# Optimization experiments

Hardware: AMD Instinct MI355X
Metric: run time of the kernel (lower is better)

Reference implementation:

```python
import jax, jax.numpy as jnp
import numpy as np

UNITS = 2048
RHO = 0.99          # spectral_radius
LEAKY = 1.0         # leaky integration coefficient
INPUT_SCALING = 1.0
BIAS_SCALING = 1.0
B, T, D_IN = 32, 512, 128


def setup_inputs() -> dict:
    key = jax.random.key(0)
    k1, k2, k3 = jax.random.split(key, 3)
    inputs = jax.random.normal(k1, (B, T, D_IN), dtype=jnp.float32)
    h0 = jnp.zeros((B, UNITS), dtype=jnp.float32)
    # original uses deterministic +/-1 signs from pi digits; same structure: sign matrix * scaling
    kernel = jnp.where(jax.random.uniform(k2, (D_IN, UNITS)) >= 0.5, 1.0, -1.0).astype(jnp.float32) * INPUT_SCALING
    bias = jnp.where(jax.random.uniform(k3, (UNITS,)) >= 0.5, 1.0, -1.0).astype(jnp.float32) * BIAS_SCALING
    return {"inputs": inputs, "h0": h0, "kernel": kernel, "bias": bias}


def reference(inputs, h0, kernel, bias):
    # Precompute input projection for all timesteps: [B, T, U]
    u = jnp.einsum("btd,du->btu", inputs, kernel)

    def step(h, u_t):
        # prev @ recurrent_kernel == spectral_radius * cyclic shift of prev
        state_part = RHO * jnp.roll(h, 1, axis=-1)
        h_new = h * (1.0 - LEAKY) + jnp.tanh(u_t + bias + state_part) * LEAKY
        return h_new, h_new

    _, ys = jax.lax.scan(step, h0, jnp.swapaxes(u, 0, 1))  # scan over time
    return jnp.swapaxes(ys, 0, 1)  # [B, T, U]
```

## Files before the change

### kernel.cpp

```cpp
#include <hip/hip_runtime.h>
#include <hip/hip_bf16.h>

#define U_ 2048
#define T_ 512
#define K_ 128
#define B_ 32
#define RHO_ 0.99f
#define CPB 128
#define NTILES 9
#define NSLOTS 10

typedef __attribute__((ext_vector_type(8))) short short8;
typedef __attribute__((ext_vector_type(4))) float f32x4;

__device__ __forceinline__ unsigned short bf16_rne(float x) {
  unsigned int u = __float_as_uint(x);
  u += 0x7FFFu + ((u >> 16) & 1u);
  return (unsigned short)(u >> 16);
}

#define GLOAD_LDS16(gsrc, ldst)                                        \
  __builtin_amdgcn_global_load_lds(                                    \
      (const __attribute__((address_space(1))) void*)(gsrc),           \
      (__attribute__((address_space(3))) void*)(ldst), 16, 0, 0)

__global__ __launch_bounds__(256) void convert_a_kernel(
    const float* __restrict__ A, unsigned short* __restrict__ Ab) {
  const int gi = blockIdx.x * 256 + threadIdx.x;
  const int m = gi >> 5;
  const int kq = (gi & 31) << 2;
  const float4 v = *(const float4*)&A[(size_t)m * K_ + kq];
  ushort4 hi, lo;
  hi.x = bf16_rne(v.x); hi.y = bf16_rne(v.y); hi.z = bf16_rne(v.z); hi.w = bf16_rne(v.w);
  lo.x = bf16_rne(v.x - __uint_as_float((unsigned)hi.x << 16));
  lo.y = bf16_rne(v.y - __uint_as_float((unsigned)hi.y << 16));
  lo.z = bf16_rne(v.z - __uint_as_float((unsigned)hi.z << 16));
  lo.w = bf16_rne(v.w - __uint_as_float((unsigned)hi.w << 16));
  *(ushort4*)&Ab[(size_t)m * 256 + kq] = hi;
  *(ushort4*)&Ab[(size_t)m * 256 + 128 + kq] = lo;
}

__global__ __launch_bounds__(256) void convert_w_kernel(
    const float* __restrict__ W, unsigned short* __restrict__ Wbt) {
  const int gi = blockIdx.x * 256 + threadIdx.x;
  const int kq = gi >> 11;
  const int n = gi & 2047;
  const int k = kq << 2;
  ushort4 w;
  w.x = bf16_rne(W[(size_t)(k + 0) * U_ + n]);
  w.y = bf16_rne(W[(size_t)(k + 1) * U_ + n]);
  w.z = bf16_rne(W[(size_t)(k + 2) * U_ + n]);
  w.w = bf16_rne(W[(size_t)(k + 3) * U_ + n]);
  *(ushort4*)&Wbt[(size_t)n * 256 + k] = w;
  *(ushort4*)&Wbt[(size_t)n * 256 + 128 + k] = w;
}

__global__ __launch_bounds__(256, 2) void fused_gemm_scan5_kernel(
    const unsigned short* __restrict__ Ab, const unsigned short* __restrict__ Wbt,
    const float* __restrict__ bias, const float* __restrict__ h0,
    float* __restrict__ out) {
  __shared__ unsigned short Wl[NSLOTS * 2048];
  __shared__ unsigned short Al[2][4096];
  __shared__ float u_lds[2][16 * 146];
  const int tid = threadIdx.x;
  const int id = blockIdx.x + (blockIdx.y << 4);
  const int xcd = id & 7;
  const int wk = id >> 3;
  const int b = (xcd << 2) + (wk >> 4);
  const int bx = wk & 15;
  const int c0 = bx << 7;
  const int cbase = bx << 3;
  const int wave = tid >> 6;
  const int lane = tid & 63;
  const int r = lane & 15;
  const int q = lane >> 4;

  const unsigned short* const aBase = Ab + (((size_t)b * T_) << 8);

  if (tid < 128) {
    #pragma unroll
    for (int k = 0; k < 4; ++k) {
      const int p = tid + (k << 7);
      const int row = p >> 5, pg = p & 31;
      GLOAD_LDS16(aBase + ((size_t)row << 8) + ((pg ^ (row & 7)) << 3),
                  &Al[0][p << 3]);
    }
    #pragma unroll
    for (int j = 0; j < NTILES; ++j) {
      const int g = (cbase + j) & 127;
      #pragma unroll
      for (int k = 0; k < 2; ++k) {
        const int p = tid + (k << 7);
        const int row = p >> 4, pg = p & 15;
        GLOAD_LDS16(Wbt + ((size_t)((g << 4) + row) << 8) + ((pg ^ (row & 7)) << 3),
                    &Wl[(j << 11) + (p << 3)]);
      }
    }
  }
  float bv[3], nbv[3];
  bv[0] = bias[(c0 + (wave << 4) + r) & (U_ - 1)];
  bv[1] = bias[(c0 + ((wave + 4) << 4) + r) & (U_ - 1)];
  bv[2] = (wave == 2) ? bias[(c0 + 128 + r) & (U_ - 1)] : 0.0f;
  float h_prev = 0.0f;
  if (tid < CPB)
    h_prev = h0[((size_t)b << 11) + ((c0 + tid + U_ - 1) & (U_ - 1))];
  float hreg[16];

  __syncthreads();

  for (int it = 0; it < T_ / 16; ++it) {
    const int cur = it & 1;
    const int t0 = it << 4;

    if (tid < 128 && it + 1 < T_ / 16) {
      #pragma unroll
      for (int k = 0; k < 4; ++k) {
        const int p = tid + (k << 7);
        const int row = p >> 5, pg = p & 31;
        GLOAD_LDS16(aBase + ((size_t)(t0 + 16 + row) << 8) + ((pg ^ (row & 7)) << 3),
                    &Al[cur ^ 1][p << 3]);
      }
      const int g = (cbase + it + NTILES) & 127;
      const int snew = (it + NTILES) % NSLOTS;
      #pragma unroll
      for (int k = 0; k < 2; ++k) {
        const int p = tid + (k << 7);
        const int row = p >> 4, pg = p & 15;
        GLOAD_LDS16(Wbt + ((size_t)((g << 4) + row) << 8) + ((pg ^ (row & 7)) << 3),
                    &Wl[(snew << 11) + (p << 3)]);
      }
    }
    if (it + 1 < T_ / 16) {
      nbv[0] = bias[(c0 + t0 + 16 + (wave << 4) + r) & (U_ - 1)];
      nbv[1] = bias[(c0 + t0 + 16 + ((wave + 4) << 4) + r) & (U_ - 1)];
      if (wave == 2) nbv[2] = bias[(c0 + t0 + 16 + 128 + r) & (U_ - 1)];
    }
    __builtin_amdgcn_sched_barrier(0);

    if (tid < CPB && it > 0) {
      const int t0p = t0 - 16;
      float* const orow = out + (((size_t)(b * T_ + t0p)) << 11);
      #pragma unroll
      for (int tt = 0; tt < 16; ++tt)
        __builtin_nontemporal_store(
            hreg[tt], &orow[((size_t)tt << 11) + ((c0 + tid + t0p + tt) & (U_ - 1))]);
    }

    short8 af[8];
    #pragma unroll
    for (int ks = 0; ks < 8; ++ks)
      af[ks] = *(const short8*)&Al[cur][(r << 8) + ((((ks << 2) + q) ^ (r & 7)) << 3)];

    #pragma unroll
    for (int u = 0; u < 3; ++u) {
      const int j = (u < 2) ? (wave + (u << 2)) : 8;
      if (u < 2 || wave == 2) {
        const int slot = (it + j) % NSLOTS;
        short8 bfk[4];
        #pragma unroll
        for (int ks = 0; ks < 4; ++ks)
          bfk[ks] = *(const short8*)&Wl[(slot << 11) + (r << 7) +
                                        ((((ks << 2) + q) ^ (r & 7)) << 3)];
        f32x4 acc = (f32x4){0.f, 0.f, 0.f, 0.f};
        #pragma unroll
        for (int ks = 0; ks < 8; ++ks)
          acc = __builtin_amdgcn_mfma_f32_16x16x32_bf16(af[ks], bfk[ks & 3], acc, 0, 0, 0);
        #pragma unroll
        for (int reg = 0; reg < 4; ++reg)
          u_lds[cur][((q << 2) + reg) * 146 + (j << 4) + r] = acc[reg] + bv[u];
      }
    }

    asm volatile("s_waitcnt vmcnt(16) lgkmcnt(0)\n\ts_barrier" ::: "memory");
    __builtin_amdgcn_sched_barrier(0);

    if (tid < CPB) {
      float uv[16];
      #pragma unroll
      for (int tt = 0; tt < 16; ++tt)
        uv[tt] = u_lds[cur][tt * 146 + tid + tt];
      float x = fmaf(RHO_, h_prev, uv[0]);
      #pragma unroll
      for (int tt = 0; tt < 16; ++tt) {
        float e = __builtin_amdgcn_exp2f(2.8853900817779268f * x);
        float rc = __builtin_amdgcn_rcpf(e + 1.0f);
        hreg[tt] = fmaf(-2.0f, rc, 1.0f);
        if (tt < 15) x = fmaf(-2.0f * RHO_, rc, uv[tt + 1] + RHO_);
      }
      h_prev = hreg[15];
    }
    bv[0] = nbv[0]; bv[1] = nbv[1]; bv[2] = nbv[2];
  }

  if (tid < CPB) {
    const int t0p = T_ - 16;
    float* const orow = out + (((size_t)(b * T_ + t0p)) << 11);
    #pragma unroll
    for (int tt = 0; tt < 16; ++tt)
      __builtin_nontemporal_store(
          hreg[tt], &orow[((size_t)tt << 11) + ((c0 + tid + t0p + tt) & (U_ - 1))]);
  }
}

__device__ __forceinline__ float fast_tanh(float x) {
  float e = __builtin_amdgcn_exp2f(2.8853900817779268f * x);
  return 1.0f - 2.0f * __builtin_amdgcn_rcpf(e + 1.0f);
}

__global__ __launch_bounds__(256) void ring_scan_kernel(
    float* __restrict__ buf, const float* __restrict__ h0) {
  const int b = blockIdx.y;
  const int c = (blockIdx.x << 8) + threadIdx.x;
  float* const base = buf + (size_t)b * (T_ * U_);
  float h = h0[((size_t)b << 11) + ((c + U_ - 1) & (U_ - 1))];
  float wA[8], wB[8];
  #pragma unroll
  for (int j = 0; j < 8; ++j)
    wA[j] = base[((size_t)j << 11) + ((c + j) & (U_ - 1))];
  for (int t0 = 0; t0 < T_; t0 += 16) {
    #pragma unroll
    for (int j = 0; j < 8; ++j) {
      const int t = t0 + 8 + j;
      wB[j] = base[((size_t)t << 11) + ((c + t) & (U_ - 1))];
    }
    #pragma unroll
    for (int j = 0; j < 8; ++j) {
      const int t = t0 + j;
      h = fast_tanh(fmaf(RHO_, h, wA[j]));
      base[((size_t)t << 11) + ((c + t) & (U_ - 1))] = h;
    }
    if (t0 + 16 < T_) {
      #pragma unroll
      for (int j = 0; j < 8; ++j) {
        const int t = t0 + 16 + j;
        wA[j] = base[((size_t)t << 11) + ((c + t) & (U_ - 1))];
      }
    }
    #pragma unroll
    for (int j = 0; j < 8; ++j) {
      const int t = t0 + 8 + j;
      h = fast_tanh(fmaf(RHO_, h, wB[j]));
      base[((size_t)t << 11) + ((c + t) & (U_ - 1))] = h;
    }
  }
}

__global__ __launch_bounds__(256, 4) void gemm_bias_kernel(
    const float* __restrict__ A, const float* __restrict__ W,
    const float* __restrict__ bias, float* __restrict__ out) {
  __shared__ float Asf[64][68];
  __shared__ float Bsf[64][64];
  const int tid = threadIdx.x;
  const int m0 = blockIdx.y << 6;
  const int n0 = blockIdx.x << 6;
  const int tx = tid & 15;
  const int ty = tid >> 4;
  float acc[4][4] = {};
  #pragma unroll
  for (int kb = 0; kb < 2; ++kb) {
    if (kb) __syncthreads();
    {
      const int c4 = tid & 15;
      const int r0 = tid >> 4;
      #pragma unroll
      for (int rr = 0; rr < 4; ++rr) {
        const int r = r0 + (rr << 4);
        const float4 v = *(const float4*)(A + (size_t)(m0 + r) * K_ + (kb << 6) + (c4 << 2));
        Asf[(c4 << 2) + 0][r] = v.x;
        Asf[(c4 << 2) + 1][r] = v.y;
        Asf[(c4 << 2) + 2][r] = v.z;
        Asf[(c4 << 2) + 3][r] = v.w;
      }
    }
    {
      const int c4 = tid & 15;
      const int r0 = tid >> 4;
      #pragma unroll
      for (int rr = 0; rr < 4; ++rr) {
        const int k = r0 + (rr << 4);
        *(float4*)&Bsf[k][c4 << 2] =
            *(const float4*)(W + (size_t)((kb << 6) + k) * U_ + n0 + (c4 << 2));
      }
    }
    __syncthreads();
    #pragma unroll 16
    for (int k = 0; k < 64; ++k) {
      const float4 a = *(const float4*)&Asf[k][ty << 2];
      const float4 b = *(const float4*)&Bsf[k][tx << 2];
      acc[0][0] = fmaf(a.x, b.x, acc[0][0]); acc[0][1] = fmaf(a.x, b.y, acc[0][1]);
      acc[0][2] = fmaf(a.x, b.z, acc[0][2]); acc[0][3] = fmaf(a.x, b.w, acc[0][3]);
      acc[1][0] = fmaf(a.y, b.x, acc[1][0]); acc[1][1] = fmaf(a.y, b.y, acc[1][1]);
      acc[1][2] = fmaf(a.y, b.z, acc[1][2]); acc[1][3] = fmaf(a.y, b.w, acc[1][3]);
      acc[2][0] = fmaf(a.z, b.x, acc[2][0]); acc[2][1] = fmaf(a.z, b.y, acc[2][1]);
      acc[2][2] = fmaf(a.z, b.z, acc[2][2]); acc[2][3] = fmaf(a.z, b.w, acc[2][3]);
      acc[3][0] = fmaf(a.w, b.x, acc[3][0]); acc[3][1] = fmaf(a.w, b.y, acc[3][1]);
      acc[3][2] = fmaf(a.w, b.z, acc[3][2]); acc[3][3] = fmaf(a.w, b.w, acc[3][3]);
    }
  }
  const float4 bv = *(const float4*)(bias + n0 + (tx << 2));
  #pragma unroll
  for (int i = 0; i < 4; ++i) {
    float4 o;
    o.x = acc[i][0] + bv.x; o.y = acc[i][1] + bv.y;
    o.z = acc[i][2] + bv.z; o.w = acc[i][3] + bv.w;
    *(float4*)(out + (size_t)(m0 + (ty << 2) + i) * U_ + n0 + (tx << 2)) = o;
  }
}

extern "C" void kernel_launch(void* const* d_in, const int* in_sizes, int n_in,
                              void* d_out, int out_size, void* d_ws, size_t ws_size,
                              hipStream_t stream) {
  const float* A    = (const float*)d_in[0];
  const float* h0   = (const float*)d_in[1];
  const float* W    = (const float*)d_in[2];
  const float* bias = (const float*)d_in[3];
  float* out = (float*)d_out;

  const size_t AB_BYTES = (size_t)B_ * T_ * 256 * 2;
  const size_t WB_BYTES = (size_t)U_ * 256 * 2;
  const size_t NEEDED = AB_BYTES + WB_BYTES;

  if (ws_size >= NEEDED) {
    unsigned short* Ab  = (unsigned short*)d_ws;
    unsigned short* Wbt = (unsigned short*)((char*)d_ws + AB_BYTES);

    convert_a_kernel<<<2048, 256, 0, stream>>>(A, Ab);
    convert_w_kernel<<<256, 256, 0, stream>>>(W, Wbt);
    dim3 fg(U_ / CPB, B_);
    fused_gemm_scan5_kernel<<<fg, 256, 0, stream>>>(Ab, Wbt, bias, h0, out);
  } else {
    dim3 gemm_grid(U_ / 64, (B_ * T_) / 64);
    gemm_bias_kernel<<<gemm_grid, 256, 0, stream>>>(A, W, bias, out);
    dim3 scan_grid(U_ / 256, B_);
    ring_scan_kernel<<<scan_grid, 256, 0, stream>>>(out, h0);
  }
}
```

Before: 193.4 us.

## Split fused GEMM-scan kernel into producer and consumer waves

```diff
diff --git a/kernel.cpp b/kernel.cpp
--- a/kernel.cpp
+++ b/kernel.cpp
@@ -9,6 +9,7 @@
 #define CPB 128
 #define NTILES 9
 #define NSLOTS 10
+#define NIT (T_ / 16)
 
 typedef __attribute__((ext_vector_type(8))) short short8;
 typedef __attribute__((ext_vector_type(4))) float f32x4;
@@ -55,7 +56,7 @@
   *(ushort4*)&Wbt[(size_t)n * 256 + 128 + k] = w;
 }
 
-__global__ __launch_bounds__(256, 2) void fused_gemm_scan5_kernel(
+__global__ __launch_bounds__(256, 2) void fused_gemm_scan6_kernel(
     const unsigned short* __restrict__ Ab, const unsigned short* __restrict__ Wbt,
     const float* __restrict__ bias, const float* __restrict__ h0,
     float* __restrict__ out) {
@@ -74,13 +75,15 @@
   const int lane = tid & 63;
   const int r = lane & 15;
   const int q = lane >> 4;
+  const bool producer = (wave >= 2);
+  const int ptid = tid & 127;
 
   const unsigned short* const aBase = Ab + (((size_t)b * T_) << 8);
 
-  if (tid < 128) {
+  if (producer) {
     #pragma unroll
     for (int k = 0; k < 4; ++k) {
-      const int p = tid + (k << 7);
+      const int p = ptid + (k << 7);
       const int row = p >> 5, pg = p & 31;
       GLOAD_LDS16(aBase + ((size_t)row << 8) + ((pg ^ (row & 7)) << 3),
                   &Al[0][p << 3]);
@@ -90,91 +93,89 @@
       const int g = (cbase + j) & 127;
       #pragma unroll
       for (int k = 0; k < 2; ++k) {
-        const int p = tid + (k << 7);
+        const int p = ptid + (k << 7);
         const int row = p >> 4, pg = p & 15;
         GLOAD_LDS16(Wbt + ((size_t)((g << 4) + row) << 8) + ((pg ^ (row & 7)) << 3),
                     &Wl[(j << 11) + (p << 3)]);
       }
     }
   }
-  float bv[3], nbv[3];
-  bv[0] = bias[(c0 + (wave << 4) + r) & (U_ - 1)];
-  bv[1] = bias[(c0 + ((wave + 4) << 4) + r) & (U_ - 1)];
-  bv[2] = (wave == 2) ? bias[(c0 + 128 + r) & (U_ - 1)] : 0.0f;
   float h_prev = 0.0f;
-  if (tid < CPB)
+  float hreg[16];
+  if (!producer)
     h_prev = h0[((size_t)b << 11) + ((c0 + tid + U_ - 1) & (U_ - 1))];
-  float hreg[16];
 
   __syncthreads();
 
-  for (int it = 0; it < T_ / 16; ++it) {
+  const int isw2 = (wave == 2) ? 1 : 0;
+
+  for (int it = 0; it < NIT; ++it) {
     const int cur = it & 1;
     const int t0 = it << 4;
 
-    if (tid < 128 && it + 1 < T_ / 16) {
-      #pragma unroll
-      for (int k = 0; k < 4; ++k) {
-        const int p = tid + (k << 7);
-        const int row = p >> 5, pg = p & 31;
-        GLOAD_LDS16(aBase + ((size_t)(t0 + 16 + row) << 8) + ((pg ^ (row & 7)) << 3),
-                    &Al[cur ^ 1][p << 3]);
-      }
-      const int g = (cbase + it + NTILES) & 127;
-      const int snew = (it + NTILES) % NSLOTS;
-      #pragma unroll
-      for (int k = 0; k < 2; ++k) {
-        const int p = tid + (k << 7);
-        const int row = p >> 4, pg = p & 15;
-        GLOAD_LDS16(Wbt + ((size_t)((g << 4) + row) << 8) + ((pg ^ (row & 7)) << 3),
-                    &Wl[(snew << 11) + (p << 3)]);
-      }
-    }
-    if (it + 1 < T_ / 16) {
-      nbv[0] = bias[(c0 + t0 + 16 + (wave << 4) + r) & (U_ - 1)];
-      nbv[1] = bias[(c0 + t0 + 16 + ((wave + 4) << 4) + r) & (U_ - 1)];
-      if (wave == 2) nbv[2] = bias[(c0 + t0 + 16 + 128 + r) & (U_ - 1)];
-    }
-    __builtin_amdgcn_sched_barrier(0);
-
-    if (tid < CPB && it > 0) {
-      const int t0p = t0 - 16;
-      float* const orow = out + (((size_t)(b * T_ + t0p)) << 11);
-      #pragma unroll
-      for (int tt = 0; tt < 16; ++tt)
-        __builtin_nontemporal_store(
-            hreg[tt], &orow[((size_t)tt << 11) + ((c0 + tid + t0p + tt) & (U_ - 1))]);
-    }
-
-    short8 af[8];
-    #pragma unroll
-    for (int ks = 0; ks < 8; ++ks)
-      af[ks] = *(const short8*)&Al[cur][(r << 8) + ((((ks << 2) + q) ^ (r & 7)) << 3)];
-
-    #pragma unroll
-    for (int u = 0; u < 3; ++u) {
-      const int j = (u < 2) ? (wave + (u << 2)) : 8;
-      if (u < 2 || wave == 2) {
-        const int slot = (it + j) % NSLOTS;
-        short8 bfk[4];
+    if (producer) {
+      if (it + 1 < NIT) {
         #pragma unroll
-        for (int ks = 0; ks < 4; ++ks)
-          bfk[ks] = *(const short8*)&Wl[(slot << 11) + (r << 7) +
-                                        ((((ks << 2) + q) ^ (r & 7)) << 3)];
-        f32x4 acc = (f32x4){0.f, 0.f, 0.f, 0.f};
+        for (int k = 0; k < 4; ++k) {
+          const int p = ptid + (k << 7);
+          const int row = p >> 5, pg = p & 31;
+          GLOAD_LDS16(aBase + ((size_t)(t0 + 16 + row) << 8) + ((pg ^ (row & 7)) << 3),
+                      &Al[cur ^ 1][p << 3]);
+        }
+        const int g = (cbase + it + NTILES) & 127;
+        const int snew = (it + NTILES) % NSLOTS;
         #pragma unroll
-        for (int ks = 0; ks < 8; ++ks)
-          acc = __builtin_amdgcn_mfma_f32_16x16x32_bf16(af[ks], bfk[ks & 3], acc, 0, 0, 0);
+        for (int k = 0; k < 2; ++k) {
+          const int p = ptid + (k << 7);
+          const int row = p >> 4, pg = p & 15;
+          GLOAD_LDS16(Wbt + ((size_t)((g << 4) + row) << 8) + ((pg ^ (row & 7)) << 3),
+                      &Wl[(snew << 11) + (p << 3)]);
+        }
+      }
+      float bvv[5];
+      #pragma unroll
+      for (int u = 0; u < 5; ++u) {
+        if (u < 4 || isw2) {
+          const int j = (u < 4) ? ((isw2 ? 0 : 4) + u) : 8;
+          bvv[u] = bias[(((cbase + it + j) & 127) << 4) + r];
+        }
+      }
+      short8 af[8];
+      #pragma unroll
+      for (int ks = 0; ks < 8; ++ks)
+        af[ks] = *(const short8*)&Al[cur][(r << 8) + ((((ks << 2) + q) ^ (r & 7)) << 3)];
+      #pragma unroll
+      for (int u = 0; u < 5; ++u) {
+        if (u < 4 || isw2) {
+          const int j = (u < 4) ? ((isw2 ? 0 : 4) + u) : 8;
+          const int slot = (it + j) % NSLOTS;
+          short8 bfk[4];
+          #pragma unroll
+          for (int ks = 0; ks < 4; ++ks)
+            bfk[ks] = *(const short8*)&Wl[(slot << 11) + (r << 7) +
+                                          ((((ks << 2) + q) ^ (r & 7)) << 3)];
+          f32x4 acc = (f32x4){0.f, 0.f, 0.f, 0.f};
+          #pragma unroll
+          for (int ks = 0; ks < 8; ++ks)
+            acc = __builtin_amdgcn_mfma_f32_16x16x32_bf16(af[ks], bfk[ks & 3], acc, 0, 0, 0);
+          #pragma unroll
+          for (int reg = 0; reg < 4; ++reg)
+            u_lds[cur][((q << 2) + reg) * 146 + (j << 4) + r] = acc[reg] + bvv[u];
+        }
+      }
+      asm volatile("s_waitcnt vmcnt(0) lgkmcnt(0)\n\ts_barrier" ::: "memory");
+      __builtin_amdgcn_sched_barrier(0);
+    } else {
+      if (it > 0) {
+        const int t0p = t0 - 16;
+        float* const orow = out + (((size_t)(b * T_ + t0p)) << 11);
         #pragma unroll
-        for (int reg = 0; reg < 4; ++reg)
-          u_lds[cur][((q << 2) + reg) * 146 + (j << 4) + r] = acc[reg] + bv[u];
-      }
-    }
-
-    asm volatile("s_waitcnt vmcnt(16) lgkmcnt(0)\n\ts_barrier" ::: "memory");
-    __builtin_amdgcn_sched_barrier(0);
-
-    if (tid < CPB) {
+        for (int tt = 0; tt < 16; ++tt)
+          __builtin_nontemporal_store(
+              hreg[tt], &orow[((size_t)tt << 11) + ((c0 + tid + t0p + tt) & (U_ - 1))]);
+      }
+      asm volatile("s_waitcnt lgkmcnt(0)\n\ts_barrier" ::: "memory");
+      __builtin_amdgcn_sched_barrier(0);
       float uv[16];
       #pragma unroll
       for (int tt = 0; tt < 16; ++tt)
@@ -189,10 +190,9 @@
       }
       h_prev = hreg[15];
     }
-    bv[0] = nbv[0]; bv[1] = nbv[1]; bv[2] = nbv[2];
-  }
-
-  if (tid < CPB) {
+  }
+
+  if (!producer) {
     const int t0p = T_ - 16;
     float* const orow = out + (((size_t)(b * T_ + t0p)) << 11);
     #pragma unroll
@@ -327,7 +327,7 @@
     convert_a_kernel<<<2048, 256, 0, stream>>>(A, Ab);
     convert_w_kernel<<<256, 256, 0, stream>>>(W, Wbt);
     dim3 fg(U_ / CPB, B_);
-    fused_gemm_scan5_kernel<<<fg, 256, 0, stream>>>(Ab, Wbt, bias, h0, out);
+    fused_gemm_scan6_kernel<<<fg, 256, 0, stream>>>(Ab, Wbt, bias, h0, out);
   } else {
     dim3 gemm_grid(U_ / 64, (B_ * T_) / 64);
     gemm_bias_kernel<<<gemm_grid, 256, 0, stream>>>(A, W, bias, out);
```

After: 182.3 us. 5.7% less time.
